# Kernel tuning notes

Hardware: AMD Instinct MI355X
Metric: run time of the kernel (lower is better)

Reference implementation:

```python
import jax, jax.numpy as jnp
import numpy as np

B = 1
E = 8388608                      # embedding size (dim 1)
NNZ = 131072                     # inhibition links
MIN_SPARSITY = 0.002
MAX_SPARSITY = 0.02
BOOST_PERCENT = 1e-8             # forward default boost_percent
MAX_ACTIVE = int(np.ceil(MAX_SPARSITY * E))    # 167773, torch uses .item() -> static
MIN_ACTIVE = int(np.floor(MIN_SPARSITY * E))   # 16777


def setup_inputs() -> dict:
    key = jax.random.key(0)
    k1, k3, k4, k5 = jax.random.split(key, 4)
    x = jax.random.normal(k1, (B, E, 1, 1), dtype=jnp.float32)
    boost_tensor = jnp.zeros((B, E, 1, 1), dtype=jnp.float32)   # initial boost state (zeros_like in module)
    inh_affector = jax.random.randint(k3, (NNZ,), 0, E, dtype=jnp.int32)
    inh_affectee = jax.random.randint(k4, (NNZ,), 0, E, dtype=jnp.int32)
    # inhibition values are negative (self-inhibition, affect_value=-0.01 scale)
    inh_values = -jax.random.uniform(k5, (NNZ,), dtype=jnp.float32) * 0.05
    return {"x": x, "boost_tensor": boost_tensor, "inh_values": inh_values,
            "inh_affector": inh_affector, "inh_affectee": inh_affectee}


def reference(x, boost_tensor, inh_values, inh_affector, inh_affectee):
    xf = x.reshape(B, E)
    bf = boost_tensor.reshape(B, E)

    # --- run_boosting: PercentClosenessBoosting (units far from max get boosted) ---
    boost_new = bf + (1.0 - xf / jnp.max(xf)) * jnp.float32(BOOST_PERCENT)
    boosted = jnp.maximum(xf, 0.0) + boost_new   # tensor_above + boost_tensor

    # --- apply_sparse_self_affector: tens[affectee] += tens[affector] * values ---
    # RHS gathered from the pre-update tensor, scatter-add onto affectee coords.
    inhibited = boosted.at[0, inh_affectee].add(boosted[0, inh_affector] * inh_values)

    # --- run_k_winners_positive: keep top max_active per row, binarize positives ---
    topv, topi = jax.lax.top_k(inhibited, MAX_ACTIVE)          # [B, K]
    rows = jnp.arange(B)[:, None]
    result = jnp.zeros((B, E), dtype=jnp.float32).at[rows, topi].set(
        (topv > 0).astype(jnp.float32))

    # --- choose_boosted_to_satisfy_minimum ---
    actually_active = jnp.sum(result)
    _, boost_idx = jax.lax.top_k(boost_new, MIN_ACTIVE)        # [B, MIN_ACTIVE]
    to_activate = jnp.ceil(jnp.float32(MIN_ACTIVE) - actually_active)
    need = actually_active < jnp.float32(MIN_ACTIVE)
    add = need & (jnp.arange(MIN_ACTIVE, dtype=jnp.float32) < to_activate)
    add = jnp.broadcast_to(add.astype(jnp.float32), (B, MIN_ACTIVE))
    out = result.at[rows, boost_idx].max(add)

    return out.reshape(B, E, 1, 1)
```

## Files before the change

kernel.cpp:

```cpp
#include <hip/hip_runtime.h>
#include <stdint.h>

#define E_SIZE   8388608
#define N4       (E_SIZE / 4)
#define NNZ_SZ   131072
#define K_ACT    167773
#define MIN_ACT  16777
#define CAP      262144
#define BCAP     2048
#define TINY_F   9.5367431640625e-7f
#define NBINS    16384
#define SHIFT1   18
#define SEL_LDS  32768


__device__ __forceinline__ unsigned int f2A(float f) {
    unsigned int u = __float_as_uint(f);
    return (u & 0x80000000u) ? ~u : (u | 0x80000000u);
}
__device__ __forceinline__ unsigned int f2D(float f) { return ~f2A(f); }
__device__ __forceinline__ float A2f(unsigned int A) {
    unsigned int u = (A & 0x80000000u) ? (A & 0x7FFFFFFFu) : ~A;
    return __uint_as_float(u);
}
__device__ __forceinline__ float D2f(unsigned int D) { return A2f(~D); }

__device__ __forceinline__ float boostedf(float v, float b, float mx) {
    return fmaxf(v, 0.0f) + (b + (1.0f - v / mx) * 1e-8f);
}
__device__ __forceinline__ unsigned int binclamp14(float v) {
    return (v < TINY_F) ? (NBINS - 1u) : (f2D(v) >> SHIFT1);
}
__device__ __forceinline__ unsigned int blo_from(float mx) {
    float tlo = 0.25f * mx;
    unsigned int b = (tlo > 0.0f) ? (f2D(tlo) >> SHIFT1) : (NBINS - 1u);
    return min(b, (unsigned int)(NBINS - 1u));
}

__device__ void block_select(const unsigned int* counts, int nbins, unsigned int Krem,
                             unsigned int* res, unsigned int* scratch) {
    int t = threadIdx.x;
    int per = nbins >> 10; if (per == 0) per = 1;
    int nth = nbins / per;
    unsigned int part = 0;
    if (t < nth)
        for (int j = 0; j < per; j++) part += counts[t * per + j];
    scratch[t] = part;
    unsigned int ws = part;
    for (int off = 32; off; off >>= 1) ws += __shfl_down(ws, off, 64);
    if ((t & 63) == 0) scratch[1024 + (t >> 6)] = ws;
    __syncthreads();
    if (t == 0) {
        unsigned int cum = 0;
        int w = 0;
        for (; w < 15; w++) {
            unsigned int s = scratch[1024 + w];
            if (cum + s >= Krem) break;
            cum += s;
        }
        int tt = w * 64, te = tt + 63;
        for (; tt < te; tt++) {
            unsigned int s = scratch[tt];
            if (cum + s >= Krem) break;
            cum += s;
        }
        int b = tt * per, be = b + per - 1;
        for (; b < be; b++) {
            unsigned int s = counts[b];
            if (cum + s >= Krem) break;
            cum += s;
        }
        res[0] = (unsigned int)b;
        res[1] = Krem - cum;
    }
    __syncthreads();
}

__global__ void __launch_bounds__(256)
k_max(const float4* __restrict__ x, unsigned int* __restrict__ pmax,
      unsigned int* __restrict__ ctrl, unsigned int* __restrict__ hist) {
    int t = threadIdx.x, blk = blockIdx.x;
    if (blk == 0 && t < 64) ctrl[t] = 0u;
    if (t < 16) hist[blk * 16 + t] = 0u;
    int tid = blk * 256 + t;
    unsigned int m = 0u;
    for (int i = tid; i < N4; i += 1024 * 256) {
        float4 v = x[i];
        m = max(m, f2A(v.x)); m = max(m, f2A(v.y));
        m = max(m, f2A(v.z)); m = max(m, f2A(v.w));
    }
    for (int off = 32; off; off >>= 1)
        m = max(m, __shfl_down(m, off, 64));
    __shared__ unsigned int sm[4];
    if ((t & 63) == 0) sm[t >> 6] = m;
    __syncthreads();
    if (t == 0) pmax[blk] = max(max(sm[0], sm[1]), max(sm[2], sm[3]));
}

__device__ __forceinline__ float reduce_pmax(const unsigned int* __restrict__ pmax,
                                             unsigned int* smax) {
    int t = threadIdx.x;
    unsigned int m = pmax[t];
    for (int off = 32; off; off >>= 1)
        m = max(m, __shfl_down(m, off, 64));
    if ((t & 63) == 0) smax[t >> 6] = m;
    __syncthreads();
    if (t == 0) {
        unsigned int r = smax[0];
        for (int i = 1; i < 16; i++) r = max(r, smax[i]);
        smax[0] = r;
    }
    __syncthreads();
    return A2f(smax[0]);
}

__device__ __forceinline__ float reduce_pmax256(const unsigned int* __restrict__ pmax,
                                                unsigned int* smax) {
    int t = threadIdx.x;
    unsigned int m = max(max(pmax[t], pmax[t + 256]),
                         max(pmax[t + 512], pmax[t + 768]));
    for (int off = 32; off; off >>= 1)
        m = max(m, __shfl_down(m, off, 64));
    if ((t & 63) == 0) smax[t >> 6] = m;
    __syncthreads();
    if (t == 0) smax[0] = max(max(smax[0], smax[1]), max(smax[2], smax[3]));
    __syncthreads();
    return A2f(smax[0]);
}

__global__ void __launch_bounds__(1024)
k_boost_hist(const float4* __restrict__ x, const float4* __restrict__ bf,
             float4* __restrict__ out, const unsigned int* __restrict__ pmax,
             unsigned int* __restrict__ hist) {
    __shared__ unsigned int h[NBINS];
    __shared__ unsigned int smax[16];
    float mx = reduce_pmax(pmax, smax);
    unsigned int b_lo = blo_from(mx);
    int t = threadIdx.x;
    for (unsigned int i = t; i <= b_lo; i += 1024) h[i] = 0u;
    __syncthreads();
    int gtid = blockIdx.x * 1024 + t;
    for (int i = gtid; i < N4; i += 512 * 1024) {
        float4 v = x[i], b = bf[i];
        float4 r;
        r.x = boostedf(v.x, b.x, mx);
        r.y = boostedf(v.y, b.y, mx);
        r.z = boostedf(v.z, b.z, mx);
        r.w = boostedf(v.w, b.w, mx);
        out[i] = r;
        #define HISTONE(c) { unsigned int bc = f2D(c) >> SHIFT1; \
            if (bc <= b_lo) atomicAdd(&h[bc], 1u); }
        HISTONE(r.x); HISTONE(r.y); HISTONE(r.z); HISTONE(r.w);
        #undef HISTONE
    }
    __syncthreads();
    for (unsigned int k = t; k <= b_lo; k += 1024) {
        unsigned int c = h[k];
        if (c) atomicAdd(&hist[k], c);
    }
}

__global__ void __launch_bounds__(256)
k_scatter(const float* __restrict__ x, const float* __restrict__ bf,
          const float* __restrict__ vals, const int* __restrict__ aff,
          const int* __restrict__ afe, float* __restrict__ out,
          const unsigned int* __restrict__ pmax) {
    __shared__ unsigned int smax[16];
    float mx = reduce_pmax256(pmax, smax);
    int i = blockIdx.x * 256 + threadIdx.x;
    int a = aff[i], e = afe[i];
    float bo = boostedf(x[a], bf[a], mx);
    atomicAdd(&out[e], bo * vals[i]);
}

__global__ void __launch_bounds__(1024)
k_markscan(float4* __restrict__ out, const unsigned int* __restrict__ hist,
           unsigned int* __restrict__ ctrl, unsigned int* __restrict__ gidx,
           unsigned int* __restrict__ gD) {
    __shared__ unsigned int scratch[1040];
    __shared__ unsigned int res[2];
    __shared__ unsigned int cidx[BCAP];
    __shared__ unsigned int cDs[BCAP];
    __shared__ unsigned int smk[16];
    __shared__ unsigned int scnt, sbase;
    int t = threadIdx.x;
    block_select(hist, NBINS, (unsigned int)K_ACT, res, scratch);
    unsigned int b1 = res[0];
    unsigned int b1p1 = min(b1 + 1u, (unsigned int)(NBINS - 1));
    if (t == 0) {
        scnt = 0;
        if (blockIdx.x == 0) atomicExch(&ctrl[32], b1);
    }
    __syncthreads();
    unsigned int mk = 0;
    int gtid = blockIdx.x * 1024 + t;
    for (int i = gtid; i < N4; i += 512 * 1024) {
        float4 f = out[i];
        float4 r;
        #define MARKONE(c, rr, comp) { \
            unsigned int bc = binclamp14(c); \
            if (bc < b1) { rr = ((c) > 0.0f) ? 1.0f : 0.0f; mk += ((c) > 0.0f) ? 1u : 0u; } \
            else { rr = 0.0f; if (bc <= b1p1) { \
                unsigned int p = atomicAdd(&scnt, 1u); \
                if (p < BCAP) { cidx[p] = (unsigned int)i * 4u + comp; cDs[p] = f2D(c); } } } }
        MARKONE(f.x, r.x, 0u); MARKONE(f.y, r.y, 1u);
        MARKONE(f.z, r.z, 2u); MARKONE(f.w, r.w, 3u);
        #undef MARKONE
        out[i] = r;
    }
    for (int off = 32; off; off >>= 1) mk += __shfl_down(mk, off, 64);
    if ((t & 63) == 0) smk[t >> 6] = mk;
    __syncthreads();
    if (t == 0) {
        unsigned int s = 0;
        for (int i = 0; i < 16; i++) s += smk[i];
        atomicAdd(&ctrl[40], s);
        unsigned int m = min(scnt, (unsigned int)BCAP);
        scnt = m;
        sbase = atomicAdd(&ctrl[7], m);
    }
    __syncthreads();
    unsigned int m = scnt, base = sbase;
    for (unsigned int i = t; i < m; i += 1024) {
        unsigned int g = base + i;
        if (g < CAP) { gidx[g] = cidx[i]; gD[g] = cDs[i]; }
    }
}

__global__ void __launch_bounds__(1024)
k_select(float* __restrict__ out, const unsigned int* __restrict__ ctrl,
         const unsigned int* __restrict__ gidx, const unsigned int* __restrict__ gD) {
    __shared__ unsigned int sD[SEL_LDS];
    __shared__ unsigned int h[1024];
    __shared__ unsigned int scratch[1040];
    __shared__ unsigned int res[2];
    __shared__ unsigned int ties[128];
    __shared__ unsigned int tcnt;
    int t = threadIdx.x;
    unsigned int nc = min(ctrl[7], (unsigned int)CAP);
    unsigned int b1 = ctrl[32];
    unsigned int marked = ctrl[40];
    unsigned int Krem = (unsigned int)K_ACT - marked;
    unsigned int kb = b1 << SHIFT1;
    unsigned int ns = min(nc, (unsigned int)SEL_LDS);

    for (unsigned int i = t; i < ns; i += 1024) sD[i] = gD[i];
    h[t] = 0u;
    if (t == 0) tcnt = 0u;
    __syncthreads();
    #define GETD(i) (((i) < ns) ? sD[(i)] : gD[(i)])

    for (unsigned int i = t; i < nc; i += 1024)
        atomicAdd(&h[(GETD(i) - kb) >> 9], 1u);
    __syncthreads();
    block_select(h, 1024, Krem, res, scratch);
    unsigned int b2 = res[0], Krem2 = res[1];

    if (t < 512) h[t] = 0u;
    __syncthreads();
    for (unsigned int i = t; i < nc; i += 1024) {
        unsigned int key = GETD(i) - kb;
        if ((key >> 9) == b2) atomicAdd(&h[key & 511u], 1u);
    }
    __syncthreads();
    block_select(h, 512, Krem2, res, scratch);
    unsigned int b3 = res[0], need = res[1];
    unsigned int T = kb + (b2 << 9) + b3;

    for (unsigned int i = t; i < nc; i += 1024) {
        if (GETD(i) == T) {
            unsigned int p = atomicAdd(&tcnt, 1u);
            if (p < 128) ties[p] = gidx[i];
        }
    }
    __syncthreads();
    unsigned int M = min(tcnt, 128u);
    float val = (D2f(T) > 0.0f) ? 1.0f : 0.0f;
    for (unsigned int i = t; i < M; i += 1024) {
        unsigned int idx = ties[i];
        unsigned int rank = 0;
        for (unsigned int j = 0; j < M; j++) rank += (ties[j] < idx) ? 1u : 0u;
        if (rank < need) out[idx] = val;
    }
    for (unsigned int i = t; i < nc; i += 1024) {
        unsigned int D = GETD(i);
        if (D < T) out[gidx[i]] = (D2f(D) > 0.0f) ? 1.0f : 0.0f;
    }
    #undef GETD
}

extern "C" void kernel_launch(void* const* d_in, const int* in_sizes, int n_in,
                              void* d_out, int out_size, void* d_ws, size_t ws_size,
                              hipStream_t stream) {
    const float* x    = (const float*)d_in[0];
    const float* bf   = (const float*)d_in[1];
    const float* vals = (const float*)d_in[2];
    const int*   aff  = (const int*)d_in[3];
    const int*   afe  = (const int*)d_in[4];
    float* out = (float*)d_out;

    unsigned int* ctrl = (unsigned int*)d_ws;
    unsigned int* pmax = (unsigned int*)((char*)d_ws + 4096);
    unsigned int* hist = (unsigned int*)((char*)d_ws + 8192);
    unsigned int* gidx = (unsigned int*)((char*)d_ws + 8192 + (size_t)NBINS * 4);
    unsigned int* gD   = (unsigned int*)((char*)d_ws + 8192 + (size_t)NBINS * 4 + (size_t)CAP * 4);

    k_max<<<1024, 256, 0, stream>>>((const float4*)x, pmax, ctrl, hist);
    k_boost_hist<<<512, 1024, 0, stream>>>((const float4*)x, (const float4*)bf,
                                           (float4*)out, pmax, hist);
    k_scatter<<<512, 256, 0, stream>>>(x, bf, vals, aff, afe, out, pmax);
    k_markscan<<<512, 1024, 0, stream>>>((float4*)out, hist, ctrl, gidx, gD);
    k_select<<<1, 1024, 0, stream>>>(out, ctrl, gidx, gD);
}
```

Baseline: 189.7 us.

## Split single-block top-k select into multi-block pass plus small tie-resolution block

Result: faster. 166.4 us, median of 2 (-12.3%).

```diff
diff --git a/kernel.cpp b/kernel.cpp
--- a/kernel.cpp
+++ b/kernel.cpp
@@ -8,10 +8,11 @@
 #define MIN_ACT  16777
 #define CAP      262144
 #define BCAP     2048
+#define TCAP     32768
 #define TINY_F   9.5367431640625e-7f
 #define NBINS    16384
 #define SHIFT1   18
-#define SEL_LDS  32768
+#define NSELA    128
 
 
 __device__ __forceinline__ unsigned int f2A(float f) {
@@ -78,10 +79,12 @@
 
 __global__ void __launch_bounds__(256)
 k_max(const float4* __restrict__ x, unsigned int* __restrict__ pmax,
-      unsigned int* __restrict__ ctrl, unsigned int* __restrict__ hist) {
+      unsigned int* __restrict__ ctrl, unsigned int* __restrict__ hist,
+      unsigned int* __restrict__ hist2) {
     int t = threadIdx.x, blk = blockIdx.x;
     if (blk == 0 && t < 64) ctrl[t] = 0u;
     if (t < 16) hist[blk * 16 + t] = 0u;
+    if (t == 16) hist2[blk] = 0u;
     int tid = blk * 256 + t;
     unsigned int m = 0u;
     for (int i = tid; i < N4; i += 1024 * 256) {
@@ -176,7 +179,7 @@
 __global__ void __launch_bounds__(1024)
 k_markscan(float4* __restrict__ out, const unsigned int* __restrict__ hist,
            unsigned int* __restrict__ ctrl, unsigned int* __restrict__ gidx,
-           unsigned int* __restrict__ gD) {
+           unsigned int* __restrict__ gD, unsigned int* __restrict__ hist2) {
     __shared__ unsigned int scratch[1040];
     __shared__ unsigned int res[2];
     __shared__ unsigned int cidx[BCAP];
@@ -187,6 +190,7 @@
     block_select(hist, NBINS, (unsigned int)K_ACT, res, scratch);
     unsigned int b1 = res[0];
     unsigned int b1p1 = min(b1 + 1u, (unsigned int)(NBINS - 1));
+    unsigned int kb = b1 << SHIFT1;
     if (t == 0) {
         scnt = 0;
         if (blockIdx.x == 0) atomicExch(&ctrl[32], b1);
@@ -202,7 +206,9 @@
             if (bc < b1) { rr = ((c) > 0.0f) ? 1.0f : 0.0f; mk += ((c) > 0.0f) ? 1u : 0u; } \
             else { rr = 0.0f; if (bc <= b1p1) { \
                 unsigned int p = atomicAdd(&scnt, 1u); \
-                if (p < BCAP) { cidx[p] = (unsigned int)i * 4u + comp; cDs[p] = f2D(c); } } } }
+                if (p < BCAP) { unsigned int Dv = f2D(c); \
+                    cidx[p] = (unsigned int)i * 4u + comp; cDs[p] = Dv; \
+                    atomicAdd(&hist2[min((Dv - kb) >> 9, 1023u)], 1u); } } } }
         MARKONE(f.x, r.x, 0u); MARKONE(f.y, r.y, 1u);
         MARKONE(f.z, r.z, 2u); MARKONE(f.w, r.w, 3u);
         #undef MARKONE
@@ -228,65 +234,72 @@
 }
 
 __global__ void __launch_bounds__(1024)
-k_select(float* __restrict__ out, const unsigned int* __restrict__ ctrl,
-         const unsigned int* __restrict__ gidx, const unsigned int* __restrict__ gD) {
-    __shared__ unsigned int sD[SEL_LDS];
-    __shared__ unsigned int h[1024];
+k_sel_a(float* __restrict__ out, const unsigned int* __restrict__ ctrl,
+        const unsigned int* __restrict__ gidx, const unsigned int* __restrict__ gD,
+        const unsigned int* __restrict__ hist2, unsigned int* __restrict__ ctrlw,
+        unsigned int* __restrict__ tidx, unsigned int* __restrict__ tD) {
+    __shared__ unsigned int scratch[1040];
+    __shared__ unsigned int res[2];
+    int t = threadIdx.x;
+    unsigned int nc = min(ctrl[7], (unsigned int)CAP);
+    if ((unsigned int)blockIdx.x * 1024u >= nc) return;
+    unsigned int kb = ctrl[32] << SHIFT1;
+    unsigned int Krem = (unsigned int)K_ACT - ctrl[40];
+    block_select(hist2, 1024, Krem, res, scratch);
+    unsigned int b2 = res[0];
+    for (unsigned int i = blockIdx.x * 1024 + t; i < nc; i += NSELA * 1024) {
+        unsigned int D = gD[i];
+        unsigned int k2 = min((D - kb) >> 9, 1023u);
+        if (k2 < b2) out[gidx[i]] = (D2f(D) > 0.0f) ? 1.0f : 0.0f;
+        else if (k2 == b2) {
+            unsigned int p = atomicAdd(&ctrlw[41], 1u);
+            if (p < TCAP) { tidx[p] = gidx[i]; tD[p] = D; }
+        }
+    }
+}
+
+__global__ void __launch_bounds__(1024)
+k_sel_b(float* __restrict__ out, const unsigned int* __restrict__ ctrl,
+        const unsigned int* __restrict__ hist2, const unsigned int* __restrict__ tidx,
+        const unsigned int* __restrict__ tD) {
+    __shared__ unsigned int h[512];
     __shared__ unsigned int scratch[1040];
     __shared__ unsigned int res[2];
     __shared__ unsigned int ties[128];
     __shared__ unsigned int tcnt;
     int t = threadIdx.x;
-    unsigned int nc = min(ctrl[7], (unsigned int)CAP);
-    unsigned int b1 = ctrl[32];
-    unsigned int marked = ctrl[40];
-    unsigned int Krem = (unsigned int)K_ACT - marked;
-    unsigned int kb = b1 << SHIFT1;
-    unsigned int ns = min(nc, (unsigned int)SEL_LDS);
-
-    for (unsigned int i = t; i < ns; i += 1024) sD[i] = gD[i];
-    h[t] = 0u;
+    unsigned int kb = ctrl[32] << SHIFT1;
+    unsigned int Krem = (unsigned int)K_ACT - ctrl[40];
+    block_select(hist2, 1024, Krem, res, scratch);
+    unsigned int b2 = res[0], Krem2 = res[1];
+    unsigned int nb = min(ctrl[41], (unsigned int)TCAP);
+    if (t < 512) h[t] = 0u;
     if (t == 0) tcnt = 0u;
     __syncthreads();
-    #define GETD(i) (((i) < ns) ? sD[(i)] : gD[(i)])
-
-    for (unsigned int i = t; i < nc; i += 1024)
-        atomicAdd(&h[(GETD(i) - kb) >> 9], 1u);
-    __syncthreads();
-    block_select(h, 1024, Krem, res, scratch);
-    unsigned int b2 = res[0], Krem2 = res[1];
-
-    if (t < 512) h[t] = 0u;
-    __syncthreads();
-    for (unsigned int i = t; i < nc; i += 1024) {
-        unsigned int key = GETD(i) - kb;
-        if ((key >> 9) == b2) atomicAdd(&h[key & 511u], 1u);
-    }
+    for (unsigned int i = t; i < nb; i += 1024)
+        atomicAdd(&h[(tD[i] - kb) & 511u], 1u);
     __syncthreads();
     block_select(h, 512, Krem2, res, scratch);
     unsigned int b3 = res[0], need = res[1];
     unsigned int T = kb + (b2 << 9) + b3;
-
-    for (unsigned int i = t; i < nc; i += 1024) {
-        if (GETD(i) == T) {
+    float val = (D2f(T) > 0.0f) ? 1.0f : 0.0f;
+    for (unsigned int i = t; i < nb; i += 1024) {
+        unsigned int D = tD[i];
+        unsigned int k3 = (D - kb) & 511u;
+        if (k3 < b3) out[tidx[i]] = (D2f(D) > 0.0f) ? 1.0f : 0.0f;
+        else if (D == T) {
             unsigned int p = atomicAdd(&tcnt, 1u);
-            if (p < 128) ties[p] = gidx[i];
+            if (p < 128) ties[p] = tidx[i];
         }
     }
     __syncthreads();
     unsigned int M = min(tcnt, 128u);
-    float val = (D2f(T) > 0.0f) ? 1.0f : 0.0f;
     for (unsigned int i = t; i < M; i += 1024) {
         unsigned int idx = ties[i];
         unsigned int rank = 0;
         for (unsigned int j = 0; j < M; j++) rank += (ties[j] < idx) ? 1u : 0u;
         if (rank < need) out[idx] = val;
     }
-    for (unsigned int i = t; i < nc; i += 1024) {
-        unsigned int D = GETD(i);
-        if (D < T) out[gidx[i]] = (D2f(D) > 0.0f) ? 1.0f : 0.0f;
-    }
-    #undef GETD
 }
 
 extern "C" void kernel_launch(void* const* d_in, const int* in_sizes, int n_in,
@@ -299,16 +312,21 @@
     const int*   afe  = (const int*)d_in[4];
     float* out = (float*)d_out;
 
-    unsigned int* ctrl = (unsigned int*)d_ws;
-    unsigned int* pmax = (unsigned int*)((char*)d_ws + 4096);
-    unsigned int* hist = (unsigned int*)((char*)d_ws + 8192);
-    unsigned int* gidx = (unsigned int*)((char*)d_ws + 8192 + (size_t)NBINS * 4);
-    unsigned int* gD   = (unsigned int*)((char*)d_ws + 8192 + (size_t)NBINS * 4 + (size_t)CAP * 4);
-
-    k_max<<<1024, 256, 0, stream>>>((const float4*)x, pmax, ctrl, hist);
+    char* w = (char*)d_ws;
+    unsigned int* ctrl  = (unsigned int*)w;
+    unsigned int* pmax  = (unsigned int*)(w + 4096);
+    unsigned int* hist  = (unsigned int*)(w + 8192);
+    unsigned int* hist2 = (unsigned int*)(w + 8192 + 65536);
+    unsigned int* gidx  = (unsigned int*)(w + 8192 + 65536 + 4096);
+    unsigned int* gD    = (unsigned int*)(w + 8192 + 65536 + 4096 + CAP * 4);
+    unsigned int* tidx  = (unsigned int*)(w + 8192 + 65536 + 4096 + 2 * CAP * 4);
+    unsigned int* tD    = (unsigned int*)(w + 8192 + 65536 + 4096 + 2 * CAP * 4 + TCAP * 4);
+
+    k_max<<<1024, 256, 0, stream>>>((const float4*)x, pmax, ctrl, hist, hist2);
     k_boost_hist<<<512, 1024, 0, stream>>>((const float4*)x, (const float4*)bf,
                                            (float4*)out, pmax, hist);
     k_scatter<<<512, 256, 0, stream>>>(x, bf, vals, aff, afe, out, pmax);
-    k_markscan<<<512, 1024, 0, stream>>>((float4*)out, hist, ctrl, gidx, gD);
-    k_select<<<1, 1024, 0, stream>>>(out, ctrl, gidx, gD);
-}
+    k_markscan<<<512, 1024, 0, stream>>>((float4*)out, hist, ctrl, gidx, gD, hist2);
+    k_sel_a<<<NSELA, 1024, 0, stream>>>(out, ctrl, gidx, gD, hist2, ctrl, tidx, tD);
+    k_sel_b<<<1, 1024, 0, stream>>>(out, ctrl, hist2, tidx, tD);
+}
```
